# Optimization experiments

Hardware: AMD Instinct MI355X
Metric: run time of the kernel (lower is better)

The kernel has to match this reference:

```python
import jax, jax.numpy as jnp
import numpy as np
import math

D_MODEL = 512
NUM_HEADS = 8
B, L = 2, 4096
EPS_NORM = 1e-8
PLASTICITY = 1.0


def setup_inputs() -> dict:
    key = jax.random.key(0)
    ks = jax.random.split(key, 6)
    D, H = D_MODEL, NUM_HEADS
    std = 1.0 / math.sqrt(D)
    x = jax.random.normal(ks[0], (B, L, D), dtype=jnp.float32)
    qkv_w = jax.random.normal(ks[1], (3 * D, D), dtype=jnp.float32) * std
    qkv_b = jnp.zeros((3 * D,), dtype=jnp.float32)
    out_w = jax.random.normal(ks[2], (D, D), dtype=jnp.float32) * std
    out_b = jnp.zeros((D,), dtype=jnp.float32)
    decay_w = jax.random.normal(ks[3], (H, D), dtype=jnp.float32) * 0.02
    decay_b = jnp.full((H,), 4.0, dtype=jnp.float32)
    norm_scale = jnp.ones((D,), dtype=jnp.float32)
    return {"x": x, "qkv_w": qkv_w, "qkv_b": qkv_b, "out_w": out_w,
            "out_b": out_b, "decay_w": decay_w, "decay_b": decay_b,
            "norm_scale": norm_scale}


def _hebbian_forward(x, qkv_w, qkv_b, out_w, out_b, decay_w, decay_b, norm_scale):
    Bsz, Lsz, D = x.shape
    H = NUM_HEADS
    E = D // H
    # QKV projection (torch Linear: y = x @ W.T + b)
    qkv = x @ qkv_w.T + qkv_b
    q, k, v = jnp.split(qkv, 3, axis=-1)
    q = q.reshape(Bsz, Lsz, H, E)
    k = k.reshape(Bsz, Lsz, H, E)
    v = v.reshape(Bsz, Lsz, H, E)
    # feature map: elu(x) + 1
    q = (jax.nn.elu(q) + 1.0) / math.sqrt(E)
    k = jax.nn.elu(k) + 1.0
    # input-dependent decay per head
    decay_logits = x @ decay_w.T + decay_b          # (B,L,H)
    lambdas = (0.9 + 0.1 * jax.nn.sigmoid(decay_logits)) * PLASTICITY
    log_lambdas = jnp.log(jnp.clip(lambdas, 1e-6))[..., None]   # (B,L,H,1)
    log_lambda_cum = jnp.clip(jnp.cumsum(log_lambdas, axis=1), -50.0, 50.0)
    decay_k = jnp.exp(-log_lambda_cum)
    decay_q = jnp.exp(log_lambda_cum)
    k_decayed = k * decay_k
    q_decayed = q * decay_q
    # outer-product memory state cumsum: (B,L,H,E,E)
    kv = jnp.einsum('blhe,blhf->blhef', k_decayed, v)
    memory_state = jnp.cumsum(kv, axis=1)
    k_sum_decayed = jnp.cumsum(k_decayed, axis=1)
    num = jnp.einsum('blhe,blhef->blhf', q_decayed, memory_state)
    den = jnp.einsum('blhe,blhe->blh', q_decayed, k_sum_decayed)[..., None] + 1e-6
    out = (num / den).reshape(Bsz, Lsz, D)
    out = out @ out_w.T + out_b
    # RMSNorm (dropout is identity in eval)
    rnorm = jax.lax.rsqrt(jnp.mean(out * out, axis=-1, keepdims=True) + EPS_NORM)
    return out * rnorm * norm_scale


def reference(x, qkv_w, qkv_b, out_w, out_b, decay_w, decay_b, norm_scale):
    return _hebbian_forward(x, qkv_w, qkv_b, out_w, out_b, decay_w, decay_b, norm_scale)
```

## Files before the change

### kernel.cpp

```cpp
#include <hip/hip_runtime.h>

typedef unsigned short u16;
typedef unsigned int u32;

#define B_ 2
#define L_ 4096
#define D_ 512
#define H_ 8
#define E_ 64
#define M_ (B_*L_)
#define TD (3*D_)
#define NCH (L_/64)
#define BH (B_*H_)

typedef short bf16x8 __attribute__((ext_vector_type(8)));
typedef float f32x4 __attribute__((ext_vector_type(4)));

__device__ __forceinline__ float bf2f(u16 u){ return __uint_as_float(((u32)u)<<16); }
__device__ __forceinline__ u16 f2bf(float f){
  u32 u = __float_as_uint(f);
  u32 r = u + 0x7FFFu + ((u>>16)&1u);
  return (u16)(r>>16);
}
__device__ __forceinline__ float elu1(float v){ return v>0.f ? v+1.f : expf(v); }

__device__ __forceinline__ void async_ld16(const u16* g, u16* l){
  __builtin_amdgcn_global_load_lds(
      (const __attribute__((address_space(1))) void*)g,
      (__attribute__((address_space(3))) void*)l, 16, 0, 0);
}

__global__ __launch_bounds__(256) void convert_kernel(const float* __restrict__ x,
    const float* __restrict__ qw, const float* __restrict__ ow,
    u16* __restrict__ xb, u16* __restrict__ qwb, u16* __restrict__ owb)
{
  int gid = blockIdx.x*256 + threadIdx.x;
  const float* src; u16* dst; int off;
  if (gid < 1048576){ src = x; dst = xb; off = gid; }
  else if (gid < 1048576+196608){ src = qw; dst = qwb; off = gid - 1048576; }
  else { src = ow; dst = owb; off = gid - 1048576 - 196608; }
  float4 v = ((const float4*)src)[off];
  ushort4 o; o.x=f2bf(v.x); o.y=f2bf(v.y); o.z=f2bf(v.z); o.w=f2bf(v.w);
  ((ushort4*)dst)[off] = o;
}

__global__ __launch_bounds__(64) void decay_ll_kernel(const float* __restrict__ x,
    const float* __restrict__ dw, const float* __restrict__ db, float* __restrict__ ll)
{
  int m = blockIdx.x;
  int lane = threadIdx.x;
  float xr[8];
  #pragma unroll
  for (int i=0;i<8;i++) xr[i] = x[(size_t)m*D_ + lane + 64*i];
  int b = m >> 12, l = m & (L_-1);
  for (int h=0; h<H_; h++){
    float acc = 0.f;
    #pragma unroll
    for (int i=0;i<8;i++) acc += xr[i]*dw[h*D_ + lane + 64*i];
    #pragma unroll
    for (int off=32; off>0; off>>=1) acc += __shfl_xor(acc, off);
    if (lane == h){
      float z = acc + db[h];
      float lam = 0.9f + 0.1f/(1.f + expf(-z));
      ll[((b*H_+h)*L_) + l] = logf(lam);
    }
  }
}

__global__ __launch_bounds__(1024) void scan_kernel(const float* __restrict__ ll,
    float* __restrict__ cb)
{
  int bh = blockIdx.x, t = threadIdx.x;
  __shared__ float part[1024];
  const float* p = ll + (size_t)bh*L_ + t*4;
  float v0=p[0], v1=p[1], v2=p[2], v3=p[3];
  float l0=v0, s1=v0+v1, s2=s1+v2, s3=s2+v3;
  part[t]=s3; __syncthreads();
  float sum = s3;
  for (int st=1; st<1024; st<<=1){
    float tv = (t>=st)? part[t-st] : 0.f;
    __syncthreads();
    sum += tv; part[t]=sum;
    __syncthreads();
  }
  float ex = sum - s3;
  float* c = cb + (size_t)bh*L_ + t*4;
  c[0]=fminf(50.f,fmaxf(-50.f,ex+l0));
  c[1]=fminf(50.f,fmaxf(-50.f,ex+s1));
  c[2]=fminf(50.f,fmaxf(-50.f,ex+s2));
  c[3]=fminf(50.f,fmaxf(-50.f,ex+s3));
}

template<bool OB>
__global__ __launch_bounds__(256) void gemm_mfma(const u16* __restrict__ A,
    const u16* __restrict__ W, const float* __restrict__ bias,
    void* __restrict__ Cv, int M, int N, int K)
{
  __shared__ u16 As[128*32];
  __shared__ u16 Bs[128*32];
  int n0 = blockIdx.x*128, m0 = blockIdx.y*128;
  int t = threadIdx.x, wave = t>>6, lane = t&63;
  int wm = (wave>>1)*64, wn = (wave&1)*64;
  f32x4 acc[4][4] = {};
  int srow = wave*32 + (lane>>2);
  int scol = (lane&3)*8;
  const u16* gA = A + (size_t)(m0+srow)*K + scol;
  const u16* gB = W + (size_t)(n0+srow)*K + scol;
  u16* lA = As + wave*1024;
  u16* lB = Bs + wave*1024;
  int q8 = (lane>>4)*8, r16 = lane&15;
  for (int k0=0; k0<K; k0+=32){
    async_ld16(gA + k0,                lA);
    async_ld16(gA + k0 + 16*(size_t)K, lA + 512);
    async_ld16(gB + k0,                lB);
    async_ld16(gB + k0 + 16*(size_t)K, lB + 512);
    __syncthreads();
    bf16x8 af[4], bfr[4];
    #pragma unroll
    for (int i=0;i<4;i++) af[i]  = *(const bf16x8*)&As[(wm + i*16 + r16)*32 + q8];
    #pragma unroll
    for (int j=0;j<4;j++) bfr[j] = *(const bf16x8*)&Bs[(wn + j*16 + r16)*32 + q8];
    #pragma unroll
    for (int i=0;i<4;i++)
      #pragma unroll
      for (int j=0;j<4;j++)
        acc[i][j] = __builtin_amdgcn_mfma_f32_16x16x32_bf16(af[i], bfr[j], acc[i][j], 0,0,0);
    __syncthreads();
  }
  #pragma unroll
  for (int i=0;i<4;i++){
    int row = m0 + wm + i*16 + (lane>>4)*4;
    #pragma unroll
    for (int j=0;j<4;j++){
      int col = n0 + wn + j*16 + r16;
      float bv = bias[col];
      #pragma unroll
      for (int r=0;r<4;r++){
        float val = acc[i][j][r] + bv;
        if (OB) ((u16*)Cv)[(size_t)(row+r)*N + col] = f2bf(val);
        else    ((float*)Cv)[(size_t)(row+r)*N + col] = val;
      }
    }
  }
}

__global__ __launch_bounds__(256) void transform_kernel(const u16* __restrict__ qkvb,
    const float* __restrict__ cb, u16* __restrict__ qb, u16* __restrict__ kb,
    u16* __restrict__ kt, u16* __restrict__ vt, float* __restrict__ ksc)
{
  int bid = blockIdx.x;
  int bh = bid >> 6, ch = bid & 63;
  int b = bh >> 3, h = bh & 7;
  __shared__ u16 Ks[64*68];
  __shared__ u16 Vs[64*68];
  __shared__ float ksr[256];
  int t = threadIdx.x;
  size_t mbase = (size_t)b*L_ + ch*64;
  #pragma unroll
  for (int i=0;i<2;i++){
    int idx = t + 256*i;
    int l = idx>>3, e0 = (idx&7)*8;
    float c = cb[(size_t)bh*L_ + ch*64 + l];
    float eqc = expf(c)*0.125f, ekc = expf(-c);
    const u16* src = qkvb + (mbase+l)*TD + h*64 + e0;
    u16 in[8], o[8];
    *(ushort4*)&in[0] = *(const ushort4*)(src);
    *(ushort4*)&in[4] = *(const ushort4*)(src+4);
    #pragma unroll
    for (int j=0;j<8;j++) o[j] = f2bf(elu1(bf2f(in[j]))*eqc);
    u16* qdst = qb + (mbase+l)*D_ + h*64 + e0;
    *(ushort4*)qdst = *(ushort4*)&o[0];
    *(ushort4*)(qdst+4) = *(ushort4*)&o[4];
    *(ushort4*)&in[0] = *(const ushort4*)(src + D_);
    *(ushort4*)&in[4] = *(const ushort4*)(src + D_ + 4);
    #pragma unroll
    for (int j=0;j<8;j++) o[j] = f2bf(elu1(bf2f(in[j]))*ekc);
    u16* kdst = kb + (mbase+l)*D_ + h*64 + e0;
    *(ushort4*)kdst = *(ushort4*)&o[0];
    *(ushort4*)(kdst+4) = *(ushort4*)&o[4];
    *(ushort4*)&Ks[l*68+e0]   = *(ushort4*)&o[0];
    *(ushort4*)&Ks[l*68+e0+4] = *(ushort4*)&o[4];
    *(ushort4*)&Vs[l*68+e0]   = *(const ushort4*)(src + 2*D_);
    *(ushort4*)&Vs[l*68+e0+4] = *(const ushort4*)(src + 2*D_ + 4);
  }
  __syncthreads();
  int e = t & 63, jq = t >> 6;
  float ksum = 0.f;
  u16 kv[16], vv[16];
  #pragma unroll
  for (int jj=0;jj<16;jj++){
    int j = jq*16+jj;
    kv[jj] = Ks[j*68 + e];
    ksum += bf2f(kv[jj]);
    vv[jj] = Vs[j*68 + e];
  }
  u16* kd = kt + ((size_t)bh*64 + e)*L_ + ch*64 + jq*16;
  u16* vd = vt + ((size_t)bh*64 + e)*L_ + ch*64 + jq*16;
  #pragma unroll
  for (int s=0;s<4;s++){
    *(ushort4*)(kd + s*4) = *(ushort4*)&kv[s*4];
    *(ushort4*)(vd + s*4) = *(ushort4*)&vv[s*4];
  }
  ksr[jq*64 + e] = ksum;
  __syncthreads();
  if (t < 64) ksc[bh*4096 + ch*64 + t] = ksr[t] + ksr[64+t] + ksr[128+t] + ksr[192+t];
}

__global__ __launch_bounds__(256) void chunk_sums_kernel(const u16* __restrict__ kt,
    const u16* __restrict__ vt, u16* __restrict__ Stc)
{
  int bid = blockIdx.x;
  int bh = bid >> 6, ch = bid & 63;
  __shared__ u16 KV[8192];
  int t = threadIdx.x, w = t>>6, lane = t&63;
  #pragma unroll
  for (int q=0;q<4;q++){
    int i8 = (w*4+q)&7;
    int kh = i8>>2;
    int row = (i8&3)*16 + (lane>>2);
    int kl = (lane&3)*8;
    const u16* g = (w<2 ? kt : vt) + ((size_t)bh*64+row)*L_ + ch*64 + kh*32 + kl;
    async_ld16(g, KV + (w*4+q)*512);
  }
  __syncthreads();
  const u16* Kl = KV;
  const u16* Vl = KV + 4096;
  int r16 = lane & 15, q8 = (lane>>4)*8;
  bf16x8 av[2];
  #pragma unroll
  for (int kh=0;kh<2;kh++)
    av[kh] = *(const bf16x8*)&Vl[(kh*64 + w*16 + r16)*32 + q8];
  f32x4 acc[4] = {};
  #pragma unroll
  for (int et=0;et<4;et++)
    #pragma unroll
    for (int kh=0;kh<2;kh++){
      bf16x8 bv = *(const bf16x8*)&Kl[(kh*64 + et*16 + r16)*32 + q8];
      acc[et] = __builtin_amdgcn_mfma_f32_16x16x32_bf16(av[kh], bv, acc[et], 0,0,0);
    }
  #pragma unroll
  for (int et=0;et<4;et++)
    #pragma unroll
    for (int r=0;r<4;r++){
      int f = w*16 + (lane>>4)*4 + r;
      int e = et*16 + r16;
      Stc[(((size_t)bh*64 + ch)*64 + f)*64 + e] = f2bf(acc[et][r]);
    }
}

__global__ __launch_bounds__(256) void chunk_prefix_kernel(u16* __restrict__ Stc,
    float* __restrict__ ksc)
{
  int gid = blockIdx.x*256 + threadIdx.x;
  int bh = gid >> 12, elem = gid & 4095;
  u16* p = Stc + (size_t)bh*262144 + elem;
  float run = 0.f;
  #pragma unroll 1
  for (int ch=0; ch<NCH; ch+=4){
    float v0 = bf2f(p[(ch+0)*4096]);
    float v1 = bf2f(p[(ch+1)*4096]);
    float v2 = bf2f(p[(ch+2)*4096]);
    float v3 = bf2f(p[(ch+3)*4096]);
    p[(ch+0)*4096] = f2bf(run); run += v0;
    p[(ch+1)*4096] = f2bf(run); run += v1;
    p[(ch+2)*4096] = f2bf(run); run += v2;
    p[(ch+3)*4096] = f2bf(run); run += v3;
  }
  if (gid < BH*64){
    int bh2 = gid >> 6, e = gid & 63;
    float* kp = ksc + bh2*4096 + e;
    float kr = 0.f;
    #pragma unroll 1
    for (int ch=0; ch<NCH; ch+=4){
      float v0=kp[(ch+0)*64], v1=kp[(ch+1)*64], v2=kp[(ch+2)*64], v3=kp[(ch+3)*64];
      kp[(ch+0)*64]=kr; kr+=v0; kp[(ch+1)*64]=kr; kr+=v1;
      kp[(ch+2)*64]=kr; kr+=v2; kp[(ch+3)*64]=kr; kr+=v3;
    }
  }
}

__global__ __launch_bounds__(256) void chunk_out_kernel(const u16* __restrict__ qb,
    const u16* __restrict__ kb, const u16* __restrict__ vt,
    const u16* __restrict__ Stc, const float* __restrict__ ksc,
    u16* __restrict__ attn)
{
  int bid = blockIdx.x;
  int bh = bid >> 6, ch = bid & 63;
  int b = bh >> 3, h = bh & 7;
  __shared__ u16 KV[16384];
  __shared__ u16 Ab[4096];
  __shared__ float kp[64], den4[256], den[64];
  int t = threadIdx.x, w = t>>6, lane = t&63;
  size_t mbase = (size_t)b*L_ + ch*64;
  #pragma unroll
  for (int q=0;q<8;q++){
    int kh = q>>2;
    int row = (q&3)*16 + (lane>>2);
    int kl = (lane&3)*8;
    const u16* g;
    if (w==0)      g = qb  + (mbase+row)*D_ + h*64 + kh*32 + kl;
    else if (w==1) g = kb  + (mbase+row)*D_ + h*64 + kh*32 + kl;
    else if (w==2) g = vt  + ((size_t)bh*64+row)*L_ + ch*64 + kh*32 + kl;
    else           g = Stc + (((size_t)bh*64+ch)*64 + row)*64 + kh*32 + kl;
    async_ld16(g, KV + w*4096 + q*512);
  }
  if (t < 64) kp[t] = ksc[bh*4096 + ch*64 + t];
  __syncthreads();
  const u16* Qs   = KV;
  const u16* Kb_s = KV + 4096;
  const u16* Vt_s = KV + 8192;
  const u16* St_s = KV + 12288;
  int r16 = lane & 15, q8 = (lane>>4)*8;
  bf16x8 aq[2];
  #pragma unroll
  for (int eh=0;eh<2;eh++)
    aq[eh] = *(const bf16x8*)&Qs[(eh*64 + w*16 + r16)*32 + q8];
  f32x4 accA[4] = {};
  #pragma unroll
  for (int jt=0;jt<4;jt++)
    #pragma unroll
    for (int eh=0;eh<2;eh++){
      bf16x8 bv = *(const bf16x8*)&Kb_s[(eh*64 + jt*16 + r16)*32 + q8];
      accA[jt] = __builtin_amdgcn_mfma_f32_16x16x32_bf16(aq[eh], bv, accA[jt], 0,0,0);
    }
  int l4 = t>>2, q4 = t&3;
  float dkp = 0.f;
  {
    int eh = q4>>1, el0 = (q4&1)*16;
    bf16x8 x1 = *(const bf16x8*)&Qs[(eh*64 + l4)*32 + el0];
    bf16x8 x2 = *(const bf16x8*)&Qs[(eh*64 + l4)*32 + el0 + 8];
    #pragma unroll
    for (int i=0;i<8;i++)
      dkp += bf2f((u16)x1[i])*kp[q4*16+i] + bf2f((u16)x2[i])*kp[q4*16+8+i];
  }
  #pragma unroll
  for (int jt=0;jt<4;jt++)
    #pragma unroll
    for (int r=0;r<4;r++){
      int lr = w*16 + ((lane>>4)<<2) + r;
      int j  = jt*16 + r16;
      Ab[((jt>>1)*64 + lr)*32 + (jt&1)*16 + r16] = (j <= lr) ? f2bf(accA[jt][r]) : (u16)0;
    }
  __syncthreads();
  float dA = 0.f;
  {
    int jh2 = q4>>1, jl0 = (q4&1)*16;
    bf16x8 y1 = *(const bf16x8*)&Ab[(jh2*64 + l4)*32 + jl0];
    bf16x8 y2 = *(const bf16x8*)&Ab[(jh2*64 + l4)*32 + jl0 + 8];
    #pragma unroll
    for (int i=0;i<8;i++) dA += bf2f((u16)y1[i]) + bf2f((u16)y2[i]);
  }
  den4[t] = dkp + dA;
  __syncthreads();
  if (t < 64) den[t] = den4[t*4] + den4[t*4+1] + den4[t*4+2] + den4[t*4+3] + 1e-6f;
  bf16x8 aA[2];
  #pragma unroll
  for (int jh=0;jh<2;jh++)
    aA[jh] = *(const bf16x8*)&Ab[(jh*64 + w*16 + r16)*32 + q8];
  f32x4 acc[4] = {};
  #pragma unroll
  for (int ft=0;ft<4;ft++){
    #pragma unroll
    for (int jh=0;jh<2;jh++){
      bf16x8 bv = *(const bf16x8*)&Vt_s[(jh*64 + ft*16 + r16)*32 + q8];
      acc[ft] = __builtin_amdgcn_mfma_f32_16x16x32_bf16(aA[jh], bv, acc[ft], 0,0,0);
    }
    #pragma unroll
    for (int eh=0;eh<2;eh++){
      bf16x8 bv = *(const bf16x8*)&St_s[(eh*64 + ft*16 + r16)*32 + q8];
      acc[ft] = __builtin_amdgcn_mfma_f32_16x16x32_bf16(aq[eh], bv, acc[ft], 0,0,0);
    }
  }
  __syncthreads();
  float inv[4];
  #pragma unroll
  for (int r=0;r<4;r++) inv[r] = 1.f / den[w*16 + ((lane>>4)<<2) + r];
  #pragma unroll
  for (int ft=0;ft<4;ft++)
    #pragma unroll
    for (int r=0;r<4;r++){
      int lr = w*16 + ((lane>>4)<<2) + r;
      attn[(mbase + lr)*D_ + h*64 + ft*16 + r16] = f2bf(acc[ft][r]*inv[r]);
    }
}

__global__ __launch_bounds__(256) void rmsnorm_kernel(const float* __restrict__ mid,
    const float* __restrict__ scale, float* __restrict__ out)
{
  int m = blockIdx.x, t = threadIdx.x;
  const float* row = mid + (size_t)m*D_;
  float v0 = row[t], v1 = row[t+256];
  float ss = v0*v0 + v1*v1;
  #pragma unroll
  for (int off=32; off>0; off>>=1) ss += __shfl_xor(ss, off);
  __shared__ float red[4];
  if ((t&63)==0) red[t>>6] = ss;
  __syncthreads();
  float tot = red[0]+red[1]+red[2]+red[3];
  float r = rsqrtf(tot*(1.f/512.f) + 1e-8f);
  out[(size_t)m*D_ + t]       = v0*r*scale[t];
  out[(size_t)m*D_ + t + 256] = v1*r*scale[t+256];
}

extern "C" void kernel_launch(void* const* d_in, const int* in_sizes, int n_in,
                              void* d_out, int out_size, void* d_ws, size_t ws_size,
                              hipStream_t stream)
{
  const float* x     = (const float*)d_in[0];
  const float* w_qkv = (const float*)d_in[1];
  const float* b_qkv = (const float*)d_in[2];
  const float* w_out = (const float*)d_in[3];
  const float* b_out = (const float*)d_in[4];
  const float* w_dec = (const float*)d_in[5];
  const float* b_dec = (const float*)d_in[6];
  const float* gnorm = (const float*)d_in[7];
  float* out = (float*)d_out;

  char* ws = (char*)d_ws;
  u16*   qkvb = (u16*)(ws);
  u16*   qb   = (u16*)(ws + 25165824);
  u16*   kb   = (u16*)(ws + 33554432);
  u16*   kt   = (u16*)(ws + 41943040);
  u16*   vt   = (u16*)(ws + 50331648);
  u16*   Stc  = (u16*)(ws + 58720256);
  float* ksc  = (float*)(ws + 67108864);
  float* ll   = (float*)(ws + 67371008);
  float* cb   = (float*)(ws + 67633152);
  u16*   xb   = (u16*)(ws + 67895296);
  u16*   qwb  = (u16*)(ws + 76283904);
  u16*   owb  = (u16*)(ws + 77856768);
  float* mid  = (float*)(ws);
  u16*   attn = kt;

  convert_kernel<<<dim3(5120), dim3(256), 0, stream>>>(x, w_qkv, w_out, xb, qwb, owb);
  decay_ll_kernel<<<dim3(M_), dim3(64), 0, stream>>>(x, w_dec, b_dec, ll);
  scan_kernel<<<dim3(BH), dim3(1024), 0, stream>>>(ll, cb);
  gemm_mfma<true><<<dim3(TD/128, M_/128), dim3(256), 0, stream>>>(xb, qwb, b_qkv, qkvb, M_, TD, D_);
  transform_kernel<<<dim3(BH*NCH), dim3(256), 0, stream>>>(qkvb, cb, qb, kb, kt, vt, ksc);
  chunk_sums_kernel<<<dim3(BH*NCH), dim3(256), 0, stream>>>(kt, vt, Stc);
  chunk_prefix_kernel<<<dim3(256), dim3(256), 0, stream>>>(Stc, ksc);
  chunk_out_kernel<<<dim3(BH*NCH), dim3(256), 0, stream>>>(qb, kb, vt, Stc, ksc, attn);
  gemm_mfma<false><<<dim3(D_/128, M_/128), dim3(256), 0, stream>>>(attn, owb, b_out, mid, M_, D_, D_);
  rmsnorm_kernel<<<dim3(M_), dim3(256), 0, stream>>>(mid, gnorm, out);
}
```

Before: 185.5 us.

## Fuse decay/convert and transform/chunk-sum kernels, use chunk-contiguous layouts, bf16 mid output

Merges the x-conversion with the decay logit computation, and merges the transform with the per-chunk KV state computation, so K and V no longer round-trip through transposed global buffers. Q, K, V^T and chunk states are now stored chunk-contiguous, giving the output kernel fully linear async loads. The scan switches to a 256-thread register/shuffle scan, the chunk prefix processes packed bf16 pairs, and the output projection writes bf16 instead of fp32 before RMSNorm. Together these cut launches and global traffic, at the cost of extra rounding of the pre-norm activations to bf16.

```diff
diff --git a/kernel.cpp b/kernel.cpp
--- a/kernel.cpp
+++ b/kernel.cpp
@@ -30,65 +30,76 @@
       (__attribute__((address_space(3))) void*)l, 16, 0, 0);
 }
 
-__global__ __launch_bounds__(256) void convert_kernel(const float* __restrict__ x,
+__global__ __launch_bounds__(256) void decay_conv_kernel(const float* __restrict__ x,
+    const float* __restrict__ dw, const float* __restrict__ db,
     const float* __restrict__ qw, const float* __restrict__ ow,
-    u16* __restrict__ xb, u16* __restrict__ qwb, u16* __restrict__ owb)
-{
-  int gid = blockIdx.x*256 + threadIdx.x;
-  const float* src; u16* dst; int off;
-  if (gid < 1048576){ src = x; dst = xb; off = gid; }
-  else if (gid < 1048576+196608){ src = qw; dst = qwb; off = gid - 1048576; }
-  else { src = ow; dst = owb; off = gid - 1048576 - 196608; }
-  float4 v = ((const float4*)src)[off];
-  ushort4 o; o.x=f2bf(v.x); o.y=f2bf(v.y); o.z=f2bf(v.z); o.w=f2bf(v.w);
-  ((ushort4*)dst)[off] = o;
-}
-
-__global__ __launch_bounds__(64) void decay_ll_kernel(const float* __restrict__ x,
-    const float* __restrict__ dw, const float* __restrict__ db, float* __restrict__ ll)
-{
-  int m = blockIdx.x;
-  int lane = threadIdx.x;
-  float xr[8];
-  #pragma unroll
-  for (int i=0;i<8;i++) xr[i] = x[(size_t)m*D_ + lane + 64*i];
-  int b = m >> 12, l = m & (L_-1);
-  for (int h=0; h<H_; h++){
-    float acc = 0.f;
-    #pragma unroll
-    for (int i=0;i<8;i++) acc += xr[i]*dw[h*D_ + lane + 64*i];
-    #pragma unroll
-    for (int off=32; off>0; off>>=1) acc += __shfl_xor(acc, off);
-    if (lane == h){
-      float z = acc + db[h];
-      float lam = 0.9f + 0.1f/(1.f + expf(-z));
-      ll[((b*H_+h)*L_) + l] = logf(lam);
-    }
-  }
-}
-
-__global__ __launch_bounds__(1024) void scan_kernel(const float* __restrict__ ll,
+    float* __restrict__ ll, u16* __restrict__ xb,
+    u16* __restrict__ qwb, u16* __restrict__ owb)
+{
+  int blk = blockIdx.x;
+  if (blk < 2048){
+    int wv = threadIdx.x>>6, lane = threadIdx.x&63;
+    int m = blk*4 + wv;
+    float xr[8];
+    #pragma unroll
+    for (int i=0;i<8;i++) xr[i] = x[(size_t)m*D_ + lane + 64*i];
+    #pragma unroll
+    for (int i=0;i<8;i++) xb[(size_t)m*D_ + lane + 64*i] = f2bf(xr[i]);
+    int b = m >> 12, l = m & (L_-1);
+    for (int h=0; h<H_; h++){
+      float acc = 0.f;
+      #pragma unroll
+      for (int i=0;i<8;i++) acc += xr[i]*dw[h*D_ + lane + 64*i];
+      #pragma unroll
+      for (int off=32; off>0; off>>=1) acc += __shfl_xor(acc, off);
+      if (lane == h){
+        float z = acc + db[h];
+        float lam = 0.9f + 0.1f/(1.f + expf(-z));
+        ll[((b*H_+h)*L_) + l] = logf(lam);
+      }
+    }
+  } else {
+    int gid = (blk-2048)*256 + threadIdx.x;
+    const float* src; u16* dst; int off;
+    if (gid < 196608){ src = qw; dst = qwb; off = gid; }
+    else { src = ow; dst = owb; off = gid - 196608; }
+    float4 v = ((const float4*)src)[off];
+    ushort4 o; o.x=f2bf(v.x); o.y=f2bf(v.y); o.z=f2bf(v.z); o.w=f2bf(v.w);
+    ((ushort4*)dst)[off] = o;
+  }
+}
+
+__global__ __launch_bounds__(256) void scan_kernel(const float* __restrict__ ll,
     float* __restrict__ cb)
 {
   int bh = blockIdx.x, t = threadIdx.x;
-  __shared__ float part[1024];
-  const float* p = ll + (size_t)bh*L_ + t*4;
-  float v0=p[0], v1=p[1], v2=p[2], v3=p[3];
-  float l0=v0, s1=v0+v1, s2=s1+v2, s3=s2+v3;
-  part[t]=s3; __syncthreads();
-  float sum = s3;
-  for (int st=1; st<1024; st<<=1){
-    float tv = (t>=st)? part[t-st] : 0.f;
-    __syncthreads();
-    sum += tv; part[t]=sum;
-    __syncthreads();
-  }
-  float ex = sum - s3;
-  float* c = cb + (size_t)bh*L_ + t*4;
-  c[0]=fminf(50.f,fmaxf(-50.f,ex+l0));
-  c[1]=fminf(50.f,fmaxf(-50.f,ex+s1));
-  c[2]=fminf(50.f,fmaxf(-50.f,ex+s2));
-  c[3]=fminf(50.f,fmaxf(-50.f,ex+s3));
+  int lane = t & 63, wv = t >> 6;
+  const float* p = ll + (size_t)bh*L_ + t*16;
+  float s[16];
+  #pragma unroll
+  for (int q=0;q<4;q++){
+    float4 v = *(const float4*)(p + q*4);
+    s[q*4+0]=v.x; s[q*4+1]=v.y; s[q*4+2]=v.z; s[q*4+3]=v.w;
+  }
+  #pragma unroll
+  for (int i=1;i<16;i++) s[i] += s[i-1];
+  float tot = s[15];
+  float ws = tot;
+  #pragma unroll
+  for (int off=1; off<64; off<<=1){
+    float tmp = __shfl_up(ws, off);
+    if (lane >= off) ws += tmp;
+  }
+  __shared__ float wsum[4];
+  if (lane == 63) wsum[wv] = ws;
+  __syncthreads();
+  float base = 0.f;
+  #pragma unroll
+  for (int w2=0; w2<3; w2++) if (w2 < wv) base += wsum[w2];
+  float ex = base + ws - tot;
+  float* c = cb + (size_t)bh*L_ + t*16;
+  #pragma unroll
+  for (int i=0;i<16;i++) c[i] = fminf(50.f, fmaxf(-50.f, ex + s[i]));
 }
 
 template<bool OB>
@@ -144,15 +155,17 @@
   }
 }
 
-__global__ __launch_bounds__(256) void transform_kernel(const u16* __restrict__ qkvb,
-    const float* __restrict__ cb, u16* __restrict__ qb, u16* __restrict__ kb,
-    u16* __restrict__ kt, u16* __restrict__ vt, float* __restrict__ ksc)
+__global__ __launch_bounds__(256) void transform_sums_kernel(const u16* __restrict__ qkvb,
+    const float* __restrict__ cb, u16* __restrict__ qc, u16* __restrict__ kc,
+    u16* __restrict__ vtc, u16* __restrict__ Stc, float* __restrict__ ksc)
 {
   int bid = blockIdx.x;
   int bh = bid >> 6, ch = bid & 63;
   int b = bh >> 3, h = bh & 7;
   __shared__ u16 Ks[64*68];
   __shared__ u16 Vs[64*68];
+  __shared__ u16 Ktl[4096];
+  __shared__ u16 Vtl[4096];
   __shared__ float ksr[256];
   int t = threadIdx.x;
   size_t mbase = (size_t)b*L_ + ch*64;
@@ -160,6 +173,7 @@
   for (int i=0;i<2;i++){
     int idx = t + 256*i;
     int l = idx>>3, e0 = (idx&7)*8;
+    int kh = e0>>5, ej = e0&31;
     float c = cb[(size_t)bh*L_ + ch*64 + l];
     float eqc = expf(c)*0.125f, ekc = expf(-c);
     const u16* src = qkvb + (mbase+l)*TD + h*64 + e0;
@@ -168,16 +182,16 @@
     *(ushort4*)&in[4] = *(const ushort4*)(src+4);
     #pragma unroll
     for (int j=0;j<8;j++) o[j] = f2bf(elu1(bf2f(in[j]))*eqc);
-    u16* qdst = qb + (mbase+l)*D_ + h*64 + e0;
-    *(ushort4*)qdst = *(ushort4*)&o[0];
-    *(ushort4*)(qdst+4) = *(ushort4*)&o[4];
+    u16* qd = qc + ((size_t)bid*2 + kh)*2048 + l*32 + ej;
+    *(ushort4*)qd = *(ushort4*)&o[0];
+    *(ushort4*)(qd+4) = *(ushort4*)&o[4];
     *(ushort4*)&in[0] = *(const ushort4*)(src + D_);
     *(ushort4*)&in[4] = *(const ushort4*)(src + D_ + 4);
     #pragma unroll
     for (int j=0;j<8;j++) o[j] = f2bf(elu1(bf2f(in[j]))*ekc);
-    u16* kdst = kb + (mbase+l)*D_ + h*64 + e0;
-    *(ushort4*)kdst = *(ushort4*)&o[0];
-    *(ushort4*)(kdst+4) = *(ushort4*)&o[4];
+    u16* kd = kc + ((size_t)bid*2 + kh)*2048 + l*32 + ej;
+    *(ushort4*)kd = *(ushort4*)&o[0];
+    *(ushort4*)(kd+4) = *(ushort4*)&o[4];
     *(ushort4*)&Ks[l*68+e0]   = *(ushort4*)&o[0];
     *(ushort4*)&Ks[l*68+e0+4] = *(ushort4*)&o[4];
     *(ushort4*)&Vs[l*68+e0]   = *(const ushort4*)(src + 2*D_);
@@ -185,102 +199,85 @@
   }
   __syncthreads();
   int e = t & 63, jq = t >> 6;
-  float ksum = 0.f;
-  u16 kv[16], vv[16];
-  #pragma unroll
-  for (int jj=0;jj<16;jj++){
-    int j = jq*16+jj;
-    kv[jj] = Ks[j*68 + e];
-    ksum += bf2f(kv[jj]);
-    vv[jj] = Vs[j*68 + e];
-  }
-  u16* kd = kt + ((size_t)bh*64 + e)*L_ + ch*64 + jq*16;
-  u16* vd = vt + ((size_t)bh*64 + e)*L_ + ch*64 + jq*16;
-  #pragma unroll
-  for (int s=0;s<4;s++){
-    *(ushort4*)(kd + s*4) = *(ushort4*)&kv[s*4];
-    *(ushort4*)(vd + s*4) = *(ushort4*)&vv[s*4];
-  }
-  ksr[jq*64 + e] = ksum;
-  __syncthreads();
-  if (t < 64) ksc[bh*4096 + ch*64 + t] = ksr[t] + ksr[64+t] + ksr[128+t] + ksr[192+t];
-}
-
-__global__ __launch_bounds__(256) void chunk_sums_kernel(const u16* __restrict__ kt,
-    const u16* __restrict__ vt, u16* __restrict__ Stc)
-{
-  int bid = blockIdx.x;
-  int bh = bid >> 6, ch = bid & 63;
-  __shared__ u16 KV[8192];
-  int t = threadIdx.x, w = t>>6, lane = t&63;
-  #pragma unroll
-  for (int q=0;q<4;q++){
-    int i8 = (w*4+q)&7;
-    int kh = i8>>2;
-    int row = (i8&3)*16 + (lane>>2);
-    int kl = (lane&3)*8;
-    const u16* g = (w<2 ? kt : vt) + ((size_t)bh*64+row)*L_ + ch*64 + kh*32 + kl;
-    async_ld16(g, KV + (w*4+q)*512);
-  }
-  __syncthreads();
-  const u16* Kl = KV;
-  const u16* Vl = KV + 4096;
+  {
+    u16 kv[16], vv[16];
+    float ksum = 0.f;
+    #pragma unroll
+    for (int jj=0;jj<16;jj++){
+      int j = jq*16+jj;
+      kv[jj] = Ks[j*68 + e];
+      ksum += bf2f(kv[jj]);
+      vv[jj] = Vs[j*68 + e];
+    }
+    int kh = jq>>1, jl = (jq&1)*16;
+    u16* kt = &Ktl[(kh*64 + e)*32 + jl];
+    u16* vt = &Vtl[(kh*64 + e)*32 + jl];
+    #pragma unroll
+    for (int s=0;s<4;s++){
+      *(ushort4*)(kt + s*4) = *(ushort4*)&kv[s*4];
+      *(ushort4*)(vt + s*4) = *(ushort4*)&vv[s*4];
+    }
+    ksr[t] = ksum;
+  }
+  __syncthreads();
+  {
+    *(uint4*)&vtc[(size_t)bid*4096 + t*8]        = *(const uint4*)&Vtl[t*8];
+    *(uint4*)&vtc[(size_t)bid*4096 + 2048 + t*8] = *(const uint4*)&Vtl[2048 + t*8];
+  }
+  int w = t>>6, lane = t&63;
   int r16 = lane & 15, q8 = (lane>>4)*8;
   bf16x8 av[2];
   #pragma unroll
   for (int kh=0;kh<2;kh++)
-    av[kh] = *(const bf16x8*)&Vl[(kh*64 + w*16 + r16)*32 + q8];
+    av[kh] = *(const bf16x8*)&Vtl[(kh*64 + w*16 + r16)*32 + q8];
   f32x4 acc[4] = {};
   #pragma unroll
   for (int et=0;et<4;et++)
     #pragma unroll
     for (int kh=0;kh<2;kh++){
-      bf16x8 bv = *(const bf16x8*)&Kl[(kh*64 + et*16 + r16)*32 + q8];
+      bf16x8 bv = *(const bf16x8*)&Ktl[(kh*64 + et*16 + r16)*32 + q8];
       acc[et] = __builtin_amdgcn_mfma_f32_16x16x32_bf16(av[kh], bv, acc[et], 0,0,0);
     }
   #pragma unroll
-  for (int et=0;et<4;et++)
+  for (int et=0;et<4;et++){
+    int eh = et>>1, el = (et&1)*16 + r16;
     #pragma unroll
     for (int r=0;r<4;r++){
       int f = w*16 + (lane>>4)*4 + r;
-      int e = et*16 + r16;
-      Stc[(((size_t)bh*64 + ch)*64 + f)*64 + e] = f2bf(acc[et][r]);
-    }
+      Stc[((size_t)bid*2 + eh)*2048 + f*32 + el] = f2bf(acc[et][r]);
+    }
+  }
+  if (t < 64) ksc[bid*64 + t] = ksr[t] + ksr[64+t] + ksr[128+t] + ksr[192+t];
 }
 
 __global__ __launch_bounds__(256) void chunk_prefix_kernel(u16* __restrict__ Stc,
     float* __restrict__ ksc)
 {
   int gid = blockIdx.x*256 + threadIdx.x;
-  int bh = gid >> 12, elem = gid & 4095;
-  u16* p = Stc + (size_t)bh*262144 + elem;
-  float run = 0.f;
-  #pragma unroll 1
-  for (int ch=0; ch<NCH; ch+=4){
-    float v0 = bf2f(p[(ch+0)*4096]);
-    float v1 = bf2f(p[(ch+1)*4096]);
-    float v2 = bf2f(p[(ch+2)*4096]);
-    float v3 = bf2f(p[(ch+3)*4096]);
-    p[(ch+0)*4096] = f2bf(run); run += v0;
-    p[(ch+1)*4096] = f2bf(run); run += v1;
-    p[(ch+2)*4096] = f2bf(run); run += v2;
-    p[(ch+3)*4096] = f2bf(run); run += v3;
+  int bh = gid >> 11, e2 = gid & 2047;
+  u32* p = (u32*)Stc + (size_t)bh*131072 + e2;
+  float r0 = 0.f, r1 = 0.f;
+  #pragma unroll 4
+  for (int ch=0; ch<NCH; ch++){
+    u32 v = p[ch*2048];
+    float lo = bf2f((u16)(v & 0xffffu));
+    float hi = bf2f((u16)(v >> 16));
+    p[ch*2048] = (u32)f2bf(r0) | ((u32)f2bf(r1) << 16);
+    r0 += lo; r1 += hi;
   }
   if (gid < BH*64){
     int bh2 = gid >> 6, e = gid & 63;
     float* kp = ksc + bh2*4096 + e;
     float kr = 0.f;
-    #pragma unroll 1
-    for (int ch=0; ch<NCH; ch+=4){
-      float v0=kp[(ch+0)*64], v1=kp[(ch+1)*64], v2=kp[(ch+2)*64], v3=kp[(ch+3)*64];
-      kp[(ch+0)*64]=kr; kr+=v0; kp[(ch+1)*64]=kr; kr+=v1;
-      kp[(ch+2)*64]=kr; kr+=v2; kp[(ch+3)*64]=kr; kr+=v3;
-    }
-  }
-}
-
-__global__ __launch_bounds__(256) void chunk_out_kernel(const u16* __restrict__ qb,
-    const u16* __restrict__ kb, const u16* __restrict__ vt,
+    #pragma unroll 4
+    for (int ch=0; ch<NCH; ch++){
+      float v = kp[ch*64]; kp[ch*64] = kr; kr += v;
+    }
+  }
+}
+
+__global__ __launch_bounds__(256) void chunk_out_kernel(const u16* __restrict__ qc,
+    const u16* __restrict__ kc, const u16* __restrict__ vtc,
     const u16* __restrict__ Stc, const float* __restrict__ ksc,
     u16* __restrict__ attn)
 {
@@ -292,19 +289,14 @@
   __shared__ float kp[64], den4[256], den[64];
   int t = threadIdx.x, w = t>>6, lane = t&63;
   size_t mbase = (size_t)b*L_ + ch*64;
-  #pragma unroll
-  for (int q=0;q<8;q++){
-    int kh = q>>2;
-    int row = (q&3)*16 + (lane>>2);
-    int kl = (lane&3)*8;
-    const u16* g;
-    if (w==0)      g = qb  + (mbase+row)*D_ + h*64 + kh*32 + kl;
-    else if (w==1) g = kb  + (mbase+row)*D_ + h*64 + kh*32 + kl;
-    else if (w==2) g = vt  + ((size_t)bh*64+row)*L_ + ch*64 + kh*32 + kl;
-    else           g = Stc + (((size_t)bh*64+ch)*64 + row)*64 + kh*32 + kl;
-    async_ld16(g, KV + w*4096 + q*512);
-  }
-  if (t < 64) kp[t] = ksc[bh*4096 + ch*64 + t];
+  const u16* srcs[4] = { qc, kc, vtc, Stc };
+  {
+    const u16* gbase = srcs[w] + (size_t)bid*4096 + lane*8;
+    #pragma unroll
+    for (int q=0;q<8;q++)
+      async_ld16(gbase + q*512, KV + w*4096 + q*512);
+  }
+  if (t < 64) kp[t] = ksc[bid*64 + t];
   __syncthreads();
   const u16* Qs   = KV;
   const u16* Kb_s = KV + 4096;
@@ -384,12 +376,12 @@
     }
 }
 
-__global__ __launch_bounds__(256) void rmsnorm_kernel(const float* __restrict__ mid,
+__global__ __launch_bounds__(256) void rmsnorm_kernel(const u16* __restrict__ mid,
     const float* __restrict__ scale, float* __restrict__ out)
 {
   int m = blockIdx.x, t = threadIdx.x;
-  const float* row = mid + (size_t)m*D_;
-  float v0 = row[t], v1 = row[t+256];
+  const u16* row = mid + (size_t)m*D_;
+  float v0 = bf2f(row[t]), v1 = bf2f(row[t+256]);
   float ss = v0*v0 + v1*v1;
   #pragma unroll
   for (int off=32; off>0; off>>=1) ss += __shfl_xor(ss, off);
@@ -418,28 +410,26 @@
 
   char* ws = (char*)d_ws;
   u16*   qkvb = (u16*)(ws);
-  u16*   qb   = (u16*)(ws + 25165824);
-  u16*   kb   = (u16*)(ws + 33554432);
-  u16*   kt   = (u16*)(ws + 41943040);
-  u16*   vt   = (u16*)(ws + 50331648);
-  u16*   Stc  = (u16*)(ws + 58720256);
-  float* ksc  = (float*)(ws + 67108864);
-  float* ll   = (float*)(ws + 67371008);
-  float* cb   = (float*)(ws + 67633152);
-  u16*   xb   = (u16*)(ws + 67895296);
-  u16*   qwb  = (u16*)(ws + 76283904);
-  u16*   owb  = (u16*)(ws + 77856768);
-  float* mid  = (float*)(ws);
-  u16*   attn = kt;
-
-  convert_kernel<<<dim3(5120), dim3(256), 0, stream>>>(x, w_qkv, w_out, xb, qwb, owb);
-  decay_ll_kernel<<<dim3(M_), dim3(64), 0, stream>>>(x, w_dec, b_dec, ll);
-  scan_kernel<<<dim3(BH), dim3(1024), 0, stream>>>(ll, cb);
+  u16*   qc   = (u16*)(ws + 25165824);
+  u16*   kc   = (u16*)(ws + 33554432);
+  u16*   vtc  = (u16*)(ws + 41943040);
+  u16*   Stc  = (u16*)(ws + 50331648);
+  float* ksc  = (float*)(ws + 58720256);
+  float* ll   = (float*)(ws + 58982400);
+  float* cb   = (float*)(ws + 59244544);
+  u16*   xb   = (u16*)(ws + 59506688);
+  u16*   qwb  = (u16*)(ws + 67895296);
+  u16*   owb  = (u16*)(ws + 69468160);
+  u16*   midb = qkvb;
+  u16*   attn = xb;
+
+  decay_conv_kernel<<<dim3(3072), dim3(256), 0, stream>>>(x, w_dec, b_dec, w_qkv, w_out,
+                                                          ll, xb, qwb, owb);
+  scan_kernel<<<dim3(BH), dim3(256), 0, stream>>>(ll, cb);
   gemm_mfma<true><<<dim3(TD/128, M_/128), dim3(256), 0, stream>>>(xb, qwb, b_qkv, qkvb, M_, TD, D_);
-  transform_kernel<<<dim3(BH*NCH), dim3(256), 0, stream>>>(qkvb, cb, qb, kb, kt, vt, ksc);
-  chunk_sums_kernel<<<dim3(BH*NCH), dim3(256), 0, stream>>>(kt, vt, Stc);
-  chunk_prefix_kernel<<<dim3(256), dim3(256), 0, stream>>>(Stc, ksc);
-  chunk_out_kernel<<<dim3(BH*NCH), dim3(256), 0, stream>>>(qb, kb, vt, Stc, ksc, attn);
-  gemm_mfma<false><<<dim3(D_/128, M_/128), dim3(256), 0, stream>>>(attn, owb, b_out, mid, M_, D_, D_);
-  rmsnorm_kernel<<<dim3(M_), dim3(256), 0, stream>>>(mid, gnorm, out);
-}
+  transform_sums_kernel<<<dim3(BH*NCH), dim3(256), 0, stream>>>(qkvb, cb, qc, kc, vtc, Stc, ksc);
+  chunk_prefix_kernel<<<dim3(128), dim3(256), 0, stream>>>(Stc, ksc);
+  chunk_out_kernel<<<dim3(BH*NCH), dim3(256), 0, stream>>>(qc, kc, vtc, Stc, ksc, attn);
+  gemm_mfma<true><<<dim3(D_/128, M_/128), dim3(256), 0, stream>>>(attn, owb, b_out, midb, M_, D_, D_);
+  rmsnorm_kernel<<<dim3(M_), dim3(256), 0, stream>>>(midb, gnorm, out);
+}
```

Result: faster. 172.0 us (-7.3%).
